# Kernel optimization log

Measured on AMD Instinct MI355X. Metric: run time of the kernel, lower is better.

The kernel has to match this reference:

```python
import jax, jax.numpy as jnp
import numpy as np

N = 65536      # flattened latent vectors (e.g. 64 images x 32x32 latents)
K = 1024       # num_embeddings (codebook size)
D = 64         # latent_dim


def setup_inputs() -> dict:
    key = jax.random.key(0)
    k_x, k_e = jax.random.split(key)
    inputs = jax.random.normal(k_x, (N, D), dtype=jnp.float32)
    # codebook initialized ~ tf.random_normal_initializer (stddev=0.05)
    embeddings = jax.random.normal(k_e, (K, D), dtype=jnp.float32) * 0.05
    return {"inputs": inputs, "embeddings": embeddings}


def reference(inputs, embeddings):
    # Pairwise L2 distances ||x_n - e_k||_2 -> [N, K].
    x_sq = jnp.sum(inputs * inputs, axis=-1, keepdims=True)        # [N, 1]
    e_sq = jnp.sum(embeddings * embeddings, axis=-1)               # [K]
    cross = inputs @ embeddings.T                                   # [N, K]
    sq_dist = x_sq + e_sq[None, :] - 2.0 * cross                    # [N, K]
    return jnp.sqrt(jnp.maximum(sq_dist, 0.0))
```

## Files before the change

kernel.cpp:

```cpp
#include <hip/hip_runtime.h>


typedef __attribute__((ext_vector_type(8))) short short8;
typedef __attribute__((ext_vector_type(4))) float floatx4;

#define LSTR 72
#define N_ROWS 65536

__device__ __forceinline__ unsigned short f2bf(float f) {
    unsigned int u = __float_as_uint(f);
    u += 0x7FFFu + ((u >> 16) & 1u);
    return (unsigned short)(u >> 16);
}
__device__ __forceinline__ float bf2f(unsigned short h) {
    return __uint_as_float(((unsigned int)h) << 16);
}

__global__ __launch_bounds__(256) void vq_fused(const float* __restrict__ X,
                                                const float* __restrict__ E,
                                                float* __restrict__ out,
                                                int Ktot) {
    __shared__ unsigned short lds[2 * 128 * LSTR];
    __shared__ alignas(16) float s_xsq[128];
    __shared__ alignas(16) float s_esq[128];

    const int tid = threadIdx.x;

    const int nxb = Ktot >> 7;
    const int cpx = gridDim.x >> 3;
    const int bid = blockIdx.x;
    const int swz = (bid & 7) * cpx + (bid >> 3);
    const int bx = swz % nxb;
    const int by = swz / nxb;
    const size_t m0 = (size_t)by * 128;
    const int n0 = bx * 128;

    unsigned short* ldsA = lds;
    unsigned short* ldsB = lds + 128 * LSTR;

    const float* gX = X + m0 * 64;
    const float* gE = E + (size_t)n0 * 64;

    float4 v[8][2];
    #pragma unroll
    for (int it = 0; it < 4; ++it) {
        const int g = it * 256 + tid;
        const int row = g >> 3, c8 = (g & 7) * 8;
        const float* p = gX + row * 64 + c8;
        v[it][0] = *(const float4*)p;
        v[it][1] = *(const float4*)(p + 4);
        const float* q = gE + row * 64 + c8;
        v[4 + it][0] = *(const float4*)q;
        v[4 + it][1] = *(const float4*)(q + 4);
    }

    #pragma unroll
    for (int half = 0; half < 2; ++half) {
        unsigned short* dst = half ? ldsB : ldsA;
        float* sq = half ? s_esq : s_xsq;
        #pragma unroll
        for (int it = 0; it < 4; ++it) {
            const int g = it * 256 + tid;
            const int row = g >> 3, c8 = (g & 7) * 8;
            const float* f = (const float*)&v[half * 4 + it][0];
            float s = 0.f;
            short8 pk;
            #pragma unroll
            for (int j = 0; j < 8; ++j) {
                const unsigned short h = f2bf(f[j]);
                const float r = bf2f(h);
                s = fmaf(r, r, s);
                pk[j] = (short)h;
            }
            *(short8*)&dst[row * LSTR + c8] = pk;
            s += __shfl_down(s, 4, 8);
            s += __shfl_down(s, 2, 8);
            s += __shfl_down(s, 1, 8);
            if ((tid & 7) == 0) sq[row] = s;
        }
    }
    __syncthreads();

    const int w = tid >> 6;
    const int lane = tid & 63;
    const int quad = lane >> 4;
    const int l16 = lane & 15;
    const int wm = (w >> 1) * 64;
    const int wn = (w & 1) * 64;

    short8 a0[4], a1[4], b0[4], b1[4];
    #pragma unroll
    for (int t = 0; t < 4; ++t) {
        const int ar = wm + t * 16 + l16;
        a0[t] = *(const short8*)&ldsA[ar * LSTR + quad * 8];
        a1[t] = *(const short8*)&ldsA[ar * LSTR + 32 + quad * 8];
        const int br = wn + t * 16 + l16;
        b0[t] = *(const short8*)&ldsB[br * LSTR + quad * 8];
        b1[t] = *(const short8*)&ldsB[br * LSTR + 32 + quad * 8];
    }

    floatx4 acc[4][4];
    #pragma unroll
    for (int i = 0; i < 4; ++i)
        #pragma unroll
        for (int j = 0; j < 4; ++j)
            acc[i][j] = (floatx4){0.f, 0.f, 0.f, 0.f};

    #pragma unroll
    for (int i = 0; i < 4; ++i)
        #pragma unroll
        for (int j = 0; j < 4; ++j) {
            acc[i][j] = __builtin_amdgcn_mfma_f32_16x16x32_bf16(b0[j], a0[i], acc[i][j], 0, 0, 0);
            acc[i][j] = __builtin_amdgcn_mfma_f32_16x16x32_bf16(b1[j], a1[i], acc[i][j], 0, 0, 0);
        }

    #pragma unroll
    for (int i = 0; i < 4; ++i) {
        const int orow = wm + i * 16 + l16;
        const float xq = s_xsq[orow];
        float* op = out + (m0 + orow) * (size_t)Ktot + n0;
        #pragma unroll
        for (int j = 0; j < 4; ++j) {
            const int ncol0 = wn + j * 16 + quad * 4;
            const floatx4 eqv = *(const floatx4*)&s_esq[ncol0];
            const floatx4 c = acc[i][j];
            floatx4 o;
            #pragma unroll
            for (int r = 0; r < 4; ++r)
                o[r] = __builtin_amdgcn_sqrtf(fmaxf(xq + eqv[r] - 2.0f * c[r], 0.0f));
            *(floatx4*)(op + ncol0) = o;
        }
    }
}

extern "C" void kernel_launch(void* const* d_in, const int* in_sizes, int n_in,
                              void* d_out, int out_size, void* d_ws, size_t ws_size,
                              hipStream_t stream) {
    const float* X = (const float*)d_in[0];
    const float* E = (const float*)d_in[1];
    float* out = (float*)d_out;
    const int K = in_sizes[1] / 64;

    const int tiles = (N_ROWS / 128) * (K / 128);
    vq_fused<<<dim3(tiles), dim3(256), 0, stream>>>(X, E, out, K);
}
```

Measured before the change: 287.0 us.

## Cut register pressure to raise occupancy with per-row-tile MFMA and epilogue

Adds a minimum-blocks hint of 4 per SM to the launch bounds. Loads X and E in two separate phases so fewer float4 staging registers are live at once. Restructures the MFMA loop so each row tile computes only 4 accumulators and writes its output right away, instead of holding all 16 accumulators until the end. The goal is more resident waves to hide global-store latency on this write-bound kernel, at the cost of less overlap between loads and compute within each wave.

```diff
diff --git a/kernel.cpp b/kernel.cpp
--- a/kernel.cpp
+++ b/kernel.cpp
@@ -16,11 +16,11 @@
     return __uint_as_float(((unsigned int)h) << 16);
 }
 
-__global__ __launch_bounds__(256) void vq_fused(const float* __restrict__ X,
-                                                const float* __restrict__ E,
-                                                float* __restrict__ out,
-                                                int Ktot) {
-    __shared__ unsigned short lds[2 * 128 * LSTR];
+__global__ __launch_bounds__(256, 4) void vq_fused(const float* __restrict__ X,
+                                                   const float* __restrict__ E,
+                                                   float* __restrict__ out,
+                                                   int Ktot) {
+    __shared__ alignas(16) unsigned short lds[2 * 128 * LSTR];
     __shared__ alignas(16) float s_xsq[128];
     __shared__ alignas(16) float s_esq[128];
 
@@ -41,28 +41,25 @@
     const float* gX = X + m0 * 64;
     const float* gE = E + (size_t)n0 * 64;
 
-    float4 v[8][2];
-    #pragma unroll
-    for (int it = 0; it < 4; ++it) {
-        const int g = it * 256 + tid;
-        const int row = g >> 3, c8 = (g & 7) * 8;
-        const float* p = gX + row * 64 + c8;
-        v[it][0] = *(const float4*)p;
-        v[it][1] = *(const float4*)(p + 4);
-        const float* q = gE + row * 64 + c8;
-        v[4 + it][0] = *(const float4*)q;
-        v[4 + it][1] = *(const float4*)(q + 4);
-    }
-
     #pragma unroll
     for (int half = 0; half < 2; ++half) {
+        const float* g = half ? gE : gX;
         unsigned short* dst = half ? ldsB : ldsA;
         float* sq = half ? s_esq : s_xsq;
+        float4 v[4][2];
         #pragma unroll
         for (int it = 0; it < 4; ++it) {
-            const int g = it * 256 + tid;
-            const int row = g >> 3, c8 = (g & 7) * 8;
-            const float* f = (const float*)&v[half * 4 + it][0];
+            const int gg = it * 256 + tid;
+            const int row = gg >> 3, c8 = (gg & 7) * 8;
+            const float* p = g + row * 64 + c8;
+            v[it][0] = *(const float4*)p;
+            v[it][1] = *(const float4*)(p + 4);
+        }
+        #pragma unroll
+        for (int it = 0; it < 4; ++it) {
+            const int gg = it * 256 + tid;
+            const int row = gg >> 3, c8 = (gg & 7) * 8;
+            const float* f = (const float*)&v[it][0];
             float s = 0.f;
             short8 pk;
             #pragma unroll
@@ -88,34 +85,29 @@
     const int wm = (w >> 1) * 64;
     const int wn = (w & 1) * 64;
 
-    short8 a0[4], a1[4], b0[4], b1[4];
+    short8 b0[4], b1[4];
     #pragma unroll
     for (int t = 0; t < 4; ++t) {
-        const int ar = wm + t * 16 + l16;
-        a0[t] = *(const short8*)&ldsA[ar * LSTR + quad * 8];
-        a1[t] = *(const short8*)&ldsA[ar * LSTR + 32 + quad * 8];
         const int br = wn + t * 16 + l16;
         b0[t] = *(const short8*)&ldsB[br * LSTR + quad * 8];
         b1[t] = *(const short8*)&ldsB[br * LSTR + 32 + quad * 8];
     }
 
-    floatx4 acc[4][4];
     #pragma unroll
-    for (int i = 0; i < 4; ++i)
-        #pragma unroll
-        for (int j = 0; j < 4; ++j)
-            acc[i][j] = (floatx4){0.f, 0.f, 0.f, 0.f};
+    for (int i = 0; i < 4; ++i) {
+        const int ar = wm + i * 16 + l16;
+        const short8 a0 = *(const short8*)&ldsA[ar * LSTR + quad * 8];
+        const short8 a1 = *(const short8*)&ldsA[ar * LSTR + 32 + quad * 8];
 
-    #pragma unroll
-    for (int i = 0; i < 4; ++i)
+        floatx4 acc[4];
         #pragma unroll
         for (int j = 0; j < 4; ++j) {
-            acc[i][j] = __builtin_amdgcn_mfma_f32_16x16x32_bf16(b0[j], a0[i], acc[i][j], 0, 0, 0);
-            acc[i][j] = __builtin_amdgcn_mfma_f32_16x16x32_bf16(b1[j], a1[i], acc[i][j], 0, 0, 0);
+            acc[j] = __builtin_amdgcn_mfma_f32_16x16x32_bf16(
+                b0[j], a0, (floatx4){0.f, 0.f, 0.f, 0.f}, 0, 0, 0);
+            acc[j] = __builtin_amdgcn_mfma_f32_16x16x32_bf16(
+                b1[j], a1, acc[j], 0, 0, 0);
         }
 
-    #pragma unroll
-    for (int i = 0; i < 4; ++i) {
         const int orow = wm + i * 16 + l16;
         const float xq = s_xsq[orow];
         float* op = out + (m0 + orow) * (size_t)Ktot + n0;
@@ -123,7 +115,7 @@
         for (int j = 0; j < 4; ++j) {
             const int ncol0 = wn + j * 16 + quad * 4;
             const floatx4 eqv = *(const floatx4*)&s_esq[ncol0];
-            const floatx4 c = acc[i][j];
+            const floatx4 c = acc[j];
             floatx4 o;
             #pragma unroll
             for (int r = 0; r < 4; ++r)
```

Result: faster. 280.5 us (-2.2%).
